# Kernel tuning notes

Hardware: AMD Instinct MI355X
Metric: run time of the kernel (lower is better)

Reference implementation:

```python
import jax, jax.numpy as jnp
import numpy as np

N = 50000      # nodes
E = 800000     # edges (before self loops)
F_IN = 50      # PPI num_features
H = 4          # heads
C = 64         # hidden per head
NC = 121       # PPI num_classes
NEG_SLOPE = 0.2


def setup_inputs() -> dict:
    key = jax.random.key(0)
    ks = jax.random.split(key, 20)
    p = lambda k, shape: (jax.random.normal(k, shape, jnp.float32) * 0.1)
    x0 = jax.random.normal(ks[0], (N, F_IN), jnp.float32)
    edge_index = jax.random.randint(ks[1], (2, E), 0, N, dtype=jnp.int64)
    return dict(
        x0=x0, edge_index=edge_index,
        W1=p(ks[2], (F_IN, H * C)), as1=p(ks[3], (H, C)), ad1=p(ks[4], (H, C)),
        res1=p(ks[5], (F_IN, H * C)), b1=jnp.zeros((H * C,), jnp.float32),
        W2=p(ks[6], (H * C, H * C)), as2=p(ks[7], (H, C)), ad2=p(ks[8], (H, C)),
        res2=p(ks[9], (H * C, H * C)), b2=jnp.zeros((H * C,), jnp.float32),
        W3=p(ks[10], (H * C, H * NC)), as3=p(ks[11], (H, NC)), ad3=p(ks[12], (H, NC)),
        res3=p(ks[13], (H * C, NC)), b3=jnp.zeros((NC,), jnp.float32),
    )


def _gat(x, src, dst, W, a_src, a_dst, resW, b, concat):
    """PyG-style GATConv with residual, self loops already in (src, dst)."""
    n = x.shape[0]
    heads, outc = a_src.shape
    h = (x @ W).reshape(n, heads, outc)                 # [N,H,C]
    al_s = (h * a_src).sum(-1)                          # [N,H]
    al_d = (h * a_dst).sum(-1)                          # [N,H]
    e = jax.nn.leaky_relu(al_s[src] + al_d[dst], NEG_SLOPE)  # [E,H]
    m = jax.ops.segment_max(e, dst, num_segments=n)     # stable softmax per dst
    ex = jnp.exp(e - m[dst])
    denom = jax.ops.segment_sum(ex, dst, num_segments=n)
    alpha = ex / denom[dst]                             # [E,H]
    out = jax.ops.segment_sum(h[src] * alpha[:, :, None], dst, num_segments=n)  # [N,H,C]
    out = out.reshape(n, heads * outc) if concat else out.mean(axis=1)
    return out + x @ resW + b


def reference(x0, edge_index,
              W1, as1, ad1, res1, b1,
              W2, as2, ad2, res2, b2,
              W3, as3, ad3, res3, b3):
    n = x0.shape[0]
    loop = jnp.arange(n, dtype=edge_index.dtype)        # add self loops (PyG default)
    src = jnp.concatenate([edge_index[0], loop])
    dst = jnp.concatenate([edge_index[1], loop])
    x1 = jax.nn.relu(_gat(x0, src, dst, W1, as1, ad1, res1, b1, True))
    x2 = jax.nn.relu(_gat(x1, src, dst, W2, as2, ad2, res2, b2, True))
    x3 = _gat(x2, src, dst, W3, as3, ad3, res3, b3, False)
    return x3
```

## Files before the change

kernel.cpp:

```cpp
#include <hip/hip_runtime.h>

#define NNODES 50000
#define NEDGES 800000
#define NTOT   (NEDGES + NNODES)
#define F_IN   50
#define KPAD1  64
#define HEADS  4
#define C1     64
#define HC1    256
#define NC     121
#define K1S    320
#define K3S    1280
#define N2S    512
#define N2X    520
#define SLOTS  128

typedef unsigned short ushort_t;
typedef __attribute__((ext_vector_type(4))) unsigned short ushort4_t;
typedef __attribute__((ext_vector_type(8))) unsigned short ushort8;
typedef __attribute__((ext_vector_type(8))) __bf16 bf16x8;
typedef __attribute__((ext_vector_type(4))) float f32x4;
typedef __attribute__((ext_vector_type(4))) int int4_t;

__device__ __forceinline__ ushort_t f2bf(float f) {
    union { float f; unsigned int u; } v; v.f = f;
    unsigned int u = v.u;
    return (ushort_t)((u + 0x7fffu + ((u >> 16) & 1u)) >> 16);
}
__device__ __forceinline__ float bf2f(ushort_t s) {
    union { unsigned int u; float f; } v; v.u = ((unsigned int)s) << 16;
    return v.f;
}
__device__ __forceinline__ float lrelu(float x) { return x > 0.f ? x : 0.2f * x; }
__device__ __forceinline__ f32x4 cvt4lo(ushort8 v) {
    f32x4 r; r[0] = bf2f(v[0]); r[1] = bf2f(v[1]); r[2] = bf2f(v[2]); r[3] = bf2f(v[3]);
    return r;
}
__device__ __forceinline__ f32x4 cvt4hi(ushort8 v) {
    f32x4 r; r[0] = bf2f(v[4]); r[1] = bf2f(v[5]); r[2] = bf2f(v[6]); r[3] = bf2f(v[7]);
    return r;
}
__device__ __forceinline__ void wave_lds_sync() {
    asm volatile("s_waitcnt lgkmcnt(0)" ::: "memory");
}

__device__ __forceinline__ void scatter_body4(int i0, const int* __restrict__ ei,
                                              int* __restrict__ cnt,
                                              int* __restrict__ csr_src) {
    #pragma unroll
    for (int u = 0; u < 4; ++u) {
        int i = i0 + u * 256;
        if (i >= NTOT) continue;
        int s, d;
        if (i < NEDGES) { s = ei[i]; d = ei[NEDGES + i]; }
        else            { s = d = i - NEDGES; }
        if ((unsigned)d >= NNODES) d = 0;
        if ((unsigned)s >= NNODES) s = 0;
        int k = atomicAdd(&cnt[d], 1);
        if (k < SLOTS) csr_src[d * SLOTS + k] = s;
    }
}

#define SZ_A (NNODES * KPAD1)
#define SZ_B (HC1 * K1S)
#define SZ_C (N2X * HC1)
#define SZ_D (N2X)
#define SZ_E (NC * K3S)
#define SZ_G (HC1 * 4)
#define PREP_TOTAL (SZ_A + SZ_B + SZ_C + SZ_D + SZ_E + 2 * SZ_G)
#define PREP_BLK ((PREP_TOTAL + 255) / 256)
#define SCAT_BLK ((NTOT + 1023) / 1024)
#define GEMV1_BLK (NNODES / 8)

__device__ void prep_body(int i,
                 const float* __restrict__ x0,
                 const float* __restrict__ W1, const float* __restrict__ res1,
                 const float* __restrict__ W2, const float* __restrict__ res2,
                 const float* __restrict__ W3, const float* __restrict__ res3,
                 const float* __restrict__ as2, const float* __restrict__ ad2,
                 const float* __restrict__ as3, const float* __restrict__ ad3,
                 const float* __restrict__ b2,
                 ushort_t* __restrict__ x0b, ushort_t* __restrict__ Bt1,
                 ushort_t* __restrict__ Bt2, ushort_t* __restrict__ Bt3,
                 float* __restrict__ bias520,
                 float* __restrict__ w_as3, float* __restrict__ w_ad3) {
    if (i < SZ_A) {
        int m = i >> 6, k = i & 63;
        x0b[i] = (k < F_IN) ? f2bf(x0[(size_t)m * F_IN + k]) : (ushort_t)0;
        return;
    }
    i -= SZ_A;
    if (i < SZ_B) {
        int c = i / K1S, kk = i - c * K1S;
        float v = 0.f;
        if (kk < 256) {
            int h = kk >> 6, k = kk & 63;
            if (k < F_IN && (c >> 6) == h) v = W1[(size_t)k * HC1 + c];
        } else {
            int k = kk - 256;
            if (k < F_IN) v = res1[(size_t)k * HC1 + c];
        }
        Bt1[i] = f2bf(v);
        return;
    }
    i -= SZ_B;
    if (i < SZ_C) {
        int c = i / HC1, k = i - c * HC1;
        float v;
        if (c < HC1) {
            v = W2[(size_t)k * HC1 + c];
        } else if (c < 512) {
            v = res2[(size_t)k * HC1 + (c - HC1)];
        } else {
            int j = c - 512;
            int h = j & 3;
            const float* a = (j < 4) ? as2 : ad2;
            float s = 0.f;
            for (int cc = 0; cc < C1; ++cc)
                s += W2[(size_t)k * HC1 + h * C1 + cc] * a[h * C1 + cc];
            v = s;
        }
        Bt2[i] = f2bf(v);
        return;
    }
    i -= SZ_C;
    if (i < SZ_D) {
        bias520[i] = (i >= HC1 && i < 512) ? b2[i - HC1] : 0.f;
        return;
    }
    i -= SZ_D;
    if (i < SZ_E) {
        int c = i / K3S, kk = i - c * K3S;
        float v;
        if (kk < 1024) {
            int h = kk >> 8, k = kk & 255;
            v = 0.25f * W3[(size_t)k * (HEADS * NC) + h * NC + c];
        } else {
            int k = kk - 1024;
            v = res3[(size_t)k * NC + c];
        }
        Bt3[i] = f2bf(v);
        return;
    }
    i -= SZ_E;
    {
        int grp = i / SZ_G, ii = i - grp * SZ_G;
        int k = ii >> 2, h = ii & 3;
        const float* a = grp ? ad3 : as3;
        float s = 0.f;
        for (int c = 0; c < NC; ++c)
            s += W3[(size_t)k * (HEADS * NC) + h * NC + c] * a[h * NC + c];
        (grp ? w_ad3 : w_as3)[ii] = s;
    }
}

__device__ void gemv1_body(int b, int tid,
                           const float* __restrict__ x0,
                           const float* __restrict__ W1,
                           const float* __restrict__ as1, const float* __restrict__ ad1,
                           float* __restrict__ als, float* __restrict__ ald,
                           float* lds_w ) {
    int k = tid >> 2, h = tid & 3;
    float s = 0.f, sd = 0.f;
    if (k < F_IN) {
        for (int c = 0; c < C1; ++c) {
            float wv = W1[(size_t)k * HC1 + h * C1 + c];
            s  += wv * as1[h * C1 + c];
            sd += wv * ad1[h * C1 + c];
        }
    }
    lds_w[k * 8 + h] = s;
    lds_w[k * 8 + 4 + h] = sd;
    __syncthreads();
    int wid = tid >> 6, lane = tid & 63;
    #pragma unroll
    for (int t = 0; t < 2; ++t) {
        int n = b * 8 + wid * 2 + t;
        float xv = (lane < F_IN) ? x0[(size_t)n * F_IN + lane] : 0.f;
        f32x4 was = *(const f32x4*)&lds_w[lane * 8];
        f32x4 wad = *(const f32x4*)&lds_w[lane * 8 + 4];
        f32x4 ps = xv * was, pd = xv * wad;
        #pragma unroll
        for (int off = 32; off; off >>= 1)
            #pragma unroll
            for (int hh = 0; hh < HEADS; ++hh) {
                ps[hh] += __shfl_xor(ps[hh], off);
                pd[hh] += __shfl_xor(pd[hh], off);
            }
        if (lane == 0) {
            *(f32x4*)&als[n * 4] = ps;
            *(f32x4*)&ald[n * 4] = pd;
        }
    }
}

__global__ __launch_bounds__(256)
void prep_scatter_gemv_kernel(const float* __restrict__ x0,
                 const float* __restrict__ W1, const float* __restrict__ res1,
                 const float* __restrict__ W2, const float* __restrict__ res2,
                 const float* __restrict__ W3, const float* __restrict__ res3,
                 const float* __restrict__ as1, const float* __restrict__ ad1,
                 const float* __restrict__ as2, const float* __restrict__ ad2,
                 const float* __restrict__ as3, const float* __restrict__ ad3,
                 const float* __restrict__ b2,
                 ushort_t* __restrict__ x0b, ushort_t* __restrict__ Bt1,
                 ushort_t* __restrict__ Bt2, ushort_t* __restrict__ Bt3,
                 float* __restrict__ bias520,
                 float* __restrict__ w_as3, float* __restrict__ w_ad3,
                 const int* __restrict__ ei, int* __restrict__ cnt,
                 int* __restrict__ csr_src,
                 float* __restrict__ als, float* __restrict__ ald) {
    __shared__ float lds_w[64 * 8];
    int b = blockIdx.x;
    if (b < PREP_BLK) {
        prep_body(b * 256 + threadIdx.x, x0, W1, res1, W2, res2, W3, res3,
                  as2, ad2, as3, ad3, b2, x0b, Bt1, Bt2, Bt3,
                  bias520, w_as3, w_ad3);
    } else if (b < PREP_BLK + SCAT_BLK) {
        scatter_body4((b - PREP_BLK) * 1024 + threadIdx.x, ei, cnt, csr_src);
    } else {
        gemv1_body(b - PREP_BLK - SCAT_BLK, threadIdx.x, x0, W1, as1, ad1,
                   als, ald, lds_w);
    }
}

#define BM 128
#define BN 128
#define BK 64
#define LDP (BK + 8)

__global__ __launch_bounds__(256)
void gemm_mfma_kernel(const ushort_t* __restrict__ A1, int lda1,
                      const ushort_t* __restrict__ A2, int lda2, int Ksplit,
                      const ushort_t* __restrict__ Bt, const float* __restrict__ bias,
                      ushort_t* __restrict__ Cb,
                      int M, int N, int K, int relu) {
    __shared__ ushort_t As[BM * LDP];
    __shared__ ushort_t Bs[BN * LDP];
    int tid = threadIdx.x;
    int lane = tid & 63;
    int wid = tid >> 6;
    int wm = (wid & 1) * 64, wn = (wid >> 1) * 64;
    int l15 = lane & 15;
    int q8 = (lane >> 4) * 8;
    int m0 = blockIdx.y * BM, n0 = blockIdx.x * BN;

    f32x4 acc[4][4] = {};

    for (int k0 = 0; k0 < K; k0 += BK) {
        #pragma unroll
        for (int it = 0; it < 4; ++it) {
            int c = tid + it * 256;
            int row = c >> 3, c8 = c & 7;
            int k = k0 + c8 * 8;
            ushort8 va = (ushort8)0;
            int gm = m0 + row;
            if (gm < M) {
                if (k < Ksplit) va = *(const ushort8*)&A1[(size_t)gm * lda1 + k];
                else            va = *(const ushort8*)&A2[(size_t)gm * lda2 + (k - Ksplit)];
            }
            *(ushort8*)&As[row * LDP + c8 * 8] = va;
            ushort8 vb = (ushort8)0;
            int gn = n0 + row;
            if (gn < N) vb = *(const ushort8*)&Bt[(size_t)gn * K + k];
            *(ushort8*)&Bs[row * LDP + c8 * 8] = vb;
        }
        __syncthreads();
        #pragma unroll
        for (int kk = 0; kk < BK; kk += 32) {
            bf16x8 af[4], bfr[4];
            #pragma unroll
            for (int mi = 0; mi < 4; ++mi)
                af[mi] = *(const bf16x8*)&As[(wm + mi * 16 + l15) * LDP + kk + q8];
            #pragma unroll
            for (int ni = 0; ni < 4; ++ni)
                bfr[ni] = *(const bf16x8*)&Bs[(wn + ni * 16 + l15) * LDP + kk + q8];
            #pragma unroll
            for (int mi = 0; mi < 4; ++mi)
                #pragma unroll
                for (int ni = 0; ni < 4; ++ni)
                    acc[mi][ni] = __builtin_amdgcn_mfma_f32_16x16x32_bf16(
                        af[mi], bfr[ni], acc[mi][ni], 0, 0, 0);
        }
        __syncthreads();
    }

    #pragma unroll
    for (int mi = 0; mi < 4; ++mi) {
        int mbase = m0 + wm + mi * 16 + (lane >> 4) * 4;
        #pragma unroll
        for (int ni = 0; ni < 4; ++ni) {
            int ncol = n0 + wn + ni * 16 + l15;
            if (ncol >= N) continue;
            float bv = bias ? bias[ncol] : 0.f;
            #pragma unroll
            for (int r = 0; r < 4; ++r) {
                int m = mbase + r;
                if (m >= M) continue;
                float v = acc[mi][ni][r] + bv;
                if (relu) v = fmaxf(v, 0.f);
                Cb[(size_t)m * N + ncol] = f2bf(v);
            }
        }
    }
}

__global__ __launch_bounds__(256)
void gemm2x_kernel(const ushort_t* __restrict__ A,
                   const ushort_t* __restrict__ Bt,
                   const float* __restrict__ bias,
                   ushort_t* __restrict__ comb,
                   float* __restrict__ als, float* __restrict__ ald,
                   int M) {
    __shared__ ushort_t As[BM * LDP];
    __shared__ ushort_t Bs[BN * LDP];
    int tid = threadIdx.x;
    int lane = tid & 63;
    int wid = tid >> 6;
    int wm = (wid & 1) * 64, wn = (wid >> 1) * 64;
    int l15 = lane & 15;
    int q8 = (lane >> 4) * 8;
    int m0 = blockIdx.y * BM, n0 = blockIdx.x * BN;

    f32x4 acc[4][4] = {};

    for (int k0 = 0; k0 < HC1; k0 += BK) {
        #pragma unroll
        for (int it = 0; it < 4; ++it) {
            int c = tid + it * 256;
            int row = c >> 3, c8 = c & 7;
            int k = k0 + c8 * 8;
            ushort8 va = (ushort8)0;
            int gm = m0 + row;
            if (gm < M) va = *(const ushort8*)&A[(size_t)gm * HC1 + k];
            *(ushort8*)&As[row * LDP + c8 * 8] = va;
            ushort8 vb = (ushort8)0;
            int gn = n0 + row;
            if (gn < N2X) vb = *(const ushort8*)&Bt[(size_t)gn * HC1 + k];
            *(ushort8*)&Bs[row * LDP + c8 * 8] = vb;
        }
        __syncthreads();
        #pragma unroll
        for (int kk = 0; kk < BK; kk += 32) {
            bf16x8 af[4], bfr[4];
            #pragma unroll
            for (int mi = 0; mi < 4; ++mi)
                af[mi] = *(const bf16x8*)&As[(wm + mi * 16 + l15) * LDP + kk + q8];
            #pragma unroll
            for (int ni = 0; ni < 4; ++ni)
                bfr[ni] = *(const bf16x8*)&Bs[(wn + ni * 16 + l15) * LDP + kk + q8];
            #pragma unroll
            for (int mi = 0; mi < 4; ++mi)
                #pragma unroll
                for (int ni = 0; ni < 4; ++ni)
                    acc[mi][ni] = __builtin_amdgcn_mfma_f32_16x16x32_bf16(
                        af[mi], bfr[ni], acc[mi][ni], 0, 0, 0);
        }
        __syncthreads();
    }

    #pragma unroll
    for (int mi = 0; mi < 4; ++mi) {
        int mbase = m0 + wm + mi * 16 + (lane >> 4) * 4;
        #pragma unroll
        for (int ni = 0; ni < 4; ++ni) {
            int ncol = n0 + wn + ni * 16 + l15;
            if (ncol >= N2X) continue;
            float bv = bias[ncol];
            #pragma unroll
            for (int r = 0; r < 4; ++r) {
                int m = mbase + r;
                if (m >= M) continue;
                float v = acc[mi][ni][r] + bv;
                if (ncol < 512) {
                    comb[(size_t)m * N2S + ncol] = f2bf(v);
                } else {
                    int j = ncol - 512;
                    if (j < 4) als[m * 4 + j] = v;
                    else       ald[m * 4 + (j - 4)] = v;
                }
            }
        }
    }
}

__global__ __launch_bounds__(256)
void gemm3s_kernel(const ushort_t* __restrict__ A1, int lda1,
                   const ushort_t* __restrict__ A2, int lda2, int Ksplit,
                   const ushort_t* __restrict__ Bt, const float* __restrict__ bias,
                   float* __restrict__ out, int M, int N, int K) {
    __shared__ ushort_t As[64 * LDP];
    __shared__ ushort_t Bs[128 * LDP];
    int tid = threadIdx.x, lane = tid & 63, wid = tid >> 6;
    int l15 = lane & 15, q8 = (lane >> 4) * 8;
    int m0 = blockIdx.x * 64;
    f32x4 c4[8] = {};
    for (int k0 = 0; k0 < K; k0 += BK) {
        #pragma unroll
        for (int it = 0; it < 2; ++it) {
            int c = tid + it * 256;
            int row = c >> 3, c8 = c & 7;
            int k = k0 + c8 * 8;
            ushort8 va = (ushort8)0;
            int gm = m0 + row;
            if (gm < M) {
                if (k < Ksplit) va = *(const ushort8*)&A1[(size_t)gm * lda1 + k];
                else            va = *(const ushort8*)&A2[(size_t)gm * lda2 + (k - Ksplit)];
            }
            *(ushort8*)&As[row * LDP + c8 * 8] = va;
        }
        #pragma unroll
        for (int it = 0; it < 4; ++it) {
            int c = tid + it * 256;
            int row = c >> 3, c8 = c & 7;
            int k = k0 + c8 * 8;
            ushort8 vb = (ushort8)0;
            if (row < N) vb = *(const ushort8*)&Bt[(size_t)row * K + k];
            *(ushort8*)&Bs[row * LDP + c8 * 8] = vb;
        }
        __syncthreads();
        #pragma unroll
        for (int kk = 0; kk < BK; kk += 32) {
            bf16x8 af = *(const bf16x8*)&As[(wid * 16 + l15) * LDP + kk + q8];
            #pragma unroll
            for (int ni = 0; ni < 8; ++ni) {
                bf16x8 bf = *(const bf16x8*)&Bs[(ni * 16 + l15) * LDP + kk + q8];
                c4[ni] = __builtin_amdgcn_mfma_f32_16x16x32_bf16(af, bf, c4[ni], 0, 0, 0);
            }
        }
        __syncthreads();
    }
    int rbase = m0 + wid * 16 + (lane >> 4) * 4;
    #pragma unroll
    for (int ni = 0; ni < 8; ++ni) {
        int col = ni * 16 + l15;
        if (col >= NC) continue;
        float bv = bias[col];
        #pragma unroll
        for (int r = 0; r < 4; ++r) {
            int m = rbase + r;
            if (m < M) out[(size_t)m * NC + col] = c4[ni][r] + bv;
        }
    }
}

#define E_CHUNK32(ROWBYTES)                                                   \
    int i = base + l;                                                         \
    int nv = end - base; if (nv > 32) nv = 32;                                \
    if (i < end) {                                                            \
        int s = csr_src[i];                                                   \
        soffw[l] = s * (ROWBYTES);                                            \
        f32x4 av = *(const f32x4*)&als[s * 4];                                \
        f32x4 e;                                                              \
        _Pragma("unroll")                                                     \
        for (int h = 0; h < HEADS; ++h) {                                     \
            e[h] = __expf(lrelu(av[h] + aldd[h]));                            \
            den4[h] += e[h];                                                  \
        }                                                                     \
        *(f32x4*)&sew[l * 4] = e;                                             \
    }                                                                         \
    wave_lds_sync();

#define DEN_REDUCE16                                                          \
    _Pragma("unroll")                                                         \
    for (int off = 16; off; off >>= 1)                                        \
        _Pragma("unroll")                                                     \
        for (int h = 0; h < HEADS; ++h)                                       \
            den4[h] += __shfl_xor(den4[h], off);

__global__ __launch_bounds__(256)
void agg1_kernel(const ushort_t* __restrict__ x0b,
                 const float* __restrict__ als, const float* __restrict__ ald,
                 const int* __restrict__ cnt, const int* __restrict__ csr_src,
                 ushort_t* __restrict__ aggx) {
    __shared__ int   soff[8][32];
    __shared__ float se[8][32 * 4];
    int tid = threadIdx.x;
    int hw = tid >> 5, l = tid & 31;
    int d = blockIdx.x * 8 + hw;
    int* soffw = soff[hw];
    float* sew = se[hw];
    int beg = d * SLOTS;
    int deg = cnt[d]; if (deg > SLOTS) deg = SLOTS;
    int end = beg + deg;
    f32x4 aldd = *(const f32x4*)&ald[d * 4];
    f32x4 den4 = (f32x4)0.f;
    f32x4 acc0 = (f32x4)0.f, acc1 = (f32x4)0.f;
    int lb = l * 4;
    for (int base = beg; base < end; base += 32) {
        E_CHUNK32(KPAD1 * 2)
        int j = 0;
        for (; j + 4 <= nv; j += 4) {
            int4_t o = *(const int4_t*)&soffw[j];
            f32x4 e0 = *(const f32x4*)&sew[j * 4];
            f32x4 e1 = *(const f32x4*)&sew[(j + 1) * 4];
            f32x4 e2 = *(const f32x4*)&sew[(j + 2) * 4];
            f32x4 e3 = *(const f32x4*)&sew[(j + 3) * 4];
            unsigned int v0 = *(const unsigned int*)((const char*)x0b + o.x + lb);
            unsigned int v1 = *(const unsigned int*)((const char*)x0b + o.y + lb);
            unsigned int v2 = *(const unsigned int*)((const char*)x0b + o.z + lb);
            unsigned int v3 = *(const unsigned int*)((const char*)x0b + o.w + lb);
            acc0 += e0 * bf2f((ushort_t)(v0 & 0xffffu)) + e1 * bf2f((ushort_t)(v1 & 0xffffu))
                  + e2 * bf2f((ushort_t)(v2 & 0xffffu)) + e3 * bf2f((ushort_t)(v3 & 0xffffu));
            acc1 += e0 * bf2f((ushort_t)(v0 >> 16)) + e1 * bf2f((ushort_t)(v1 >> 16))
                  + e2 * bf2f((ushort_t)(v2 >> 16)) + e3 * bf2f((ushort_t)(v3 >> 16));
        }
        for (; j < nv; ++j) {
            int o = soffw[j];
            f32x4 e = *(const f32x4*)&sew[j * 4];
            unsigned int v = *(const unsigned int*)((const char*)x0b + o + lb);
            acc0 += e * bf2f((ushort_t)(v & 0xffffu));
            acc1 += e * bf2f((ushort_t)(v >> 16));
        }
        wave_lds_sync();
    }
    DEN_REDUCE16
    #pragma unroll
    for (int h = 0; h < HEADS; ++h) {
        float r = 1.f / den4[h];
        unsigned int pk = (unsigned int)f2bf(acc0[h] * r)
                        | ((unsigned int)f2bf(acc1[h] * r) << 16);
        *(unsigned int*)&aggx[(size_t)d * HC1 + h * 64 + l * 2] = pk;
    }
}

__global__ __launch_bounds__(256)
void agg2_kernel(const ushort_t* __restrict__ comb,
                 const float* __restrict__ als, const float* __restrict__ ald,
                 const int* __restrict__ cnt, const int* __restrict__ csr_src,
                 const float* __restrict__ w_as3, const float* __restrict__ w_ad3,
                 ushort_t* __restrict__ xnext,
                 float* __restrict__ als3, float* __restrict__ ald3) {
    __shared__ int   soff[8][32];
    __shared__ float se[8][32 * 4];
    int tid = threadIdx.x;
    int hw = tid >> 5, l = tid & 31;
    int d = blockIdx.x * 8 + hw;
    int* soffw = soff[hw];
    float* sew = se[hw];
    int hh = l >> 3;
    int beg = d * SLOTS;
    int deg = cnt[d]; if (deg > SLOTS) deg = SLOTS;
    int end = beg + deg;
    f32x4 aldd = *(const f32x4*)&ald[d * 4];
    f32x4 den4 = (f32x4)0.f;
    f32x4 acc[2] = {};
    int lb = l * 16;
    for (int base = beg; base < end; base += 32) {
        E_CHUNK32(N2S * 2)
        int j = 0;
        for (; j + 4 <= nv; j += 4) {
            int4_t o = *(const int4_t*)&soffw[j];
            ushort8 v0 = *(const ushort8*)((const char*)comb + o.x + lb);
            ushort8 v1 = *(const ushort8*)((const char*)comb + o.y + lb);
            ushort8 v2 = *(const ushort8*)((const char*)comb + o.z + lb);
            ushort8 v3 = *(const ushort8*)((const char*)comb + o.w + lb);
            float e0 = sew[j * 4 + hh], e1 = sew[(j + 1) * 4 + hh];
            float e2 = sew[(j + 2) * 4 + hh], e3 = sew[(j + 3) * 4 + hh];
            acc[0] += e0 * cvt4lo(v0) + e1 * cvt4lo(v1) + e2 * cvt4lo(v2) + e3 * cvt4lo(v3);
            acc[1] += e0 * cvt4hi(v0) + e1 * cvt4hi(v1) + e2 * cvt4hi(v2) + e3 * cvt4hi(v3);
        }
        for (; j < nv; ++j) {
            int o = soffw[j];
            float e = sew[j * 4 + hh];
            ushort8 v = *(const ushort8*)((const char*)comb + o + lb);
            acc[0] += e * cvt4lo(v);
            acc[1] += e * cvt4hi(v);
        }
        wave_lds_sync();
    }
    DEN_REDUCE16
    float r = 1.f / den4[hh];
    ushort8 rv = *(const ushort8*)&comb[(size_t)d * N2S + 256 + l * 8];
    float vout[8];
    ushort8 o8;
    #pragma unroll
    for (int q = 0; q < 2; ++q)
        #pragma unroll
        for (int c = 0; c < 4; ++c) {
            float vv = fmaxf(acc[q][c] * r + bf2f(rv[q * 4 + c]), 0.f);
            vout[q * 4 + c] = vv;
            o8[q * 4 + c] = f2bf(vv);
        }
    *(ushort8*)&xnext[(size_t)d * HC1 + l * 8] = o8;
    f32x4 ps = (f32x4)0.f, pd = (f32x4)0.f;
    #pragma unroll
    for (int cc = 0; cc < 8; ++cc) {
        int col = l * 8 + cc;
        f32x4 wsj = *(const f32x4*)&w_as3[col * 4];
        f32x4 wdj = *(const f32x4*)&w_ad3[col * 4];
        ps += vout[cc] * wsj;
        pd += vout[cc] * wdj;
    }
    #pragma unroll
    for (int off = 16; off; off >>= 1) {
        #pragma unroll
        for (int h = 0; h < HEADS; ++h) {
            ps[h] += __shfl_xor(ps[h], off);
            pd[h] += __shfl_xor(pd[h], off);
        }
    }
    if (l == 0) {
        *(f32x4*)&als3[d * 4] = ps;
        *(f32x4*)&ald3[d * 4] = pd;
    }
}

__global__ __launch_bounds__(256)
void agg3_kernel(const ushort_t* __restrict__ x2b,
                 const float* __restrict__ als, const float* __restrict__ ald,
                 const int* __restrict__ cnt, const int* __restrict__ csr_src,
                 ushort_t* __restrict__ aggx) {
    __shared__ int   soff[8][32];
    __shared__ float se[8][32 * 4];
    int tid = threadIdx.x;
    int hw = tid >> 5, l = tid & 31;
    int d = blockIdx.x * 8 + hw;
    int* soffw = soff[hw];
    float* sew = se[hw];
    int beg = d * SLOTS;
    int deg = cnt[d]; if (deg > SLOTS) deg = SLOTS;
    int end = beg + deg;
    f32x4 aldd = *(const f32x4*)&ald[d * 4];
    f32x4 den4 = (f32x4)0.f;
    f32x4 acc[HEADS][2] = {};
    int lb = l * 16;
    for (int base = beg; base < end; base += 32) {
        E_CHUNK32(HC1 * 2)
        int j = 0;
        for (; j + 4 <= nv; j += 4) {
            int4_t o = *(const int4_t*)&soffw[j];
            ushort8 v0 = *(const ushort8*)((const char*)x2b + o.x + lb);
            ushort8 v1 = *(const ushort8*)((const char*)x2b + o.y + lb);
            ushort8 v2 = *(const ushort8*)((const char*)x2b + o.z + lb);
            ushort8 v3 = *(const ushort8*)((const char*)x2b + o.w + lb);
            f32x4 e0 = *(const f32x4*)&sew[j * 4];
            f32x4 e1 = *(const f32x4*)&sew[(j + 1) * 4];
            f32x4 e2 = *(const f32x4*)&sew[(j + 2) * 4];
            f32x4 e3 = *(const f32x4*)&sew[(j + 3) * 4];
            f32x4 xl, xh;
            xl = cvt4lo(v0); xh = cvt4hi(v0);
            #pragma unroll
            for (int h = 0; h < HEADS; ++h) { acc[h][0] += e0[h] * xl; acc[h][1] += e0[h] * xh; }
            xl = cvt4lo(v1); xh = cvt4hi(v1);
            #pragma unroll
            for (int h = 0; h < HEADS; ++h) { acc[h][0] += e1[h] * xl; acc[h][1] += e1[h] * xh; }
            xl = cvt4lo(v2); xh = cvt4hi(v2);
            #pragma unroll
            for (int h = 0; h < HEADS; ++h) { acc[h][0] += e2[h] * xl; acc[h][1] += e2[h] * xh; }
            xl = cvt4lo(v3); xh = cvt4hi(v3);
            #pragma unroll
            for (int h = 0; h < HEADS; ++h) { acc[h][0] += e3[h] * xl; acc[h][1] += e3[h] * xh; }
        }
        for (; j < nv; ++j) {
            int o = soffw[j];
            f32x4 e = *(const f32x4*)&sew[j * 4];
            ushort8 v = *(const ushort8*)((const char*)x2b + o + lb);
            f32x4 xl = cvt4lo(v), xh = cvt4hi(v);
            #pragma unroll
            for (int h = 0; h < HEADS; ++h) { acc[h][0] += e[h] * xl; acc[h][1] += e[h] * xh; }
        }
        wave_lds_sync();
    }
    DEN_REDUCE16
    #pragma unroll
    for (int h = 0; h < HEADS; ++h) {
        float rdv = 1.f / den4[h];
        ushort8 ow;
        #pragma unroll
        for (int q = 0; q < 2; ++q)
            #pragma unroll
            for (int c = 0; c < 4; ++c)
                ow[q * 4 + c] = f2bf(acc[h][q][c] * rdv);
        *(ushort8*)&aggx[(size_t)d * 1024 + h * HC1 + l * 8] = ow;
    }
}

extern "C" void kernel_launch(void* const* d_in, const int* in_sizes, int n_in,
                              void* d_out, int out_size, void* d_ws, size_t ws_size,
                              hipStream_t stream) {
    const float* x0   = (const float*)d_in[0];
    const int*   ei   = (const int*)d_in[1];
    const float* W1   = (const float*)d_in[2];
    const float* as1  = (const float*)d_in[3];
    const float* ad1  = (const float*)d_in[4];
    const float* res1 = (const float*)d_in[5];
    const float* b1   = (const float*)d_in[6];
    const float* W2   = (const float*)d_in[7];
    const float* as2  = (const float*)d_in[8];
    const float* ad2  = (const float*)d_in[9];
    const float* res2 = (const float*)d_in[10];
    const float* b2   = (const float*)d_in[11];
    const float* W3   = (const float*)d_in[12];
    const float* as3  = (const float*)d_in[13];
    const float* ad3  = (const float*)d_in[14];
    const float* res3 = (const float*)d_in[15];
    const float* b3   = (const float*)d_in[16];

    char* p = (char*)d_ws;
    auto alloc = [&](size_t bytes) -> void* {
        void* r = (void*)p;
        p += (bytes + 255) & ~(size_t)255;
        return r;
    };
    int*      cnt     = (int*)alloc((size_t)NNODES * 4);
    int*      csr_src = (int*)alloc((size_t)NNODES * SLOTS * 4);
    float*    als     = (float*)alloc((size_t)NNODES * HEADS * 4);
    float*    ald     = (float*)alloc((size_t)NNODES * HEADS * 4);
    float*    als3    = (float*)alloc((size_t)NNODES * HEADS * 4);
    float*    ald3    = (float*)alloc((size_t)NNODES * HEADS * 4);
    ushort_t* x0b     = (ushort_t*)alloc((size_t)NNODES * KPAD1 * 2);
    ushort_t* x2      = (ushort_t*)alloc((size_t)NNODES * HC1 * 2);
    ushort_t* Bt1     = (ushort_t*)alloc((size_t)HC1 * K1S * 2);
    ushort_t* Bt2     = (ushort_t*)alloc((size_t)N2X * HC1 * 2);
    float*    bias520 = (float*)alloc((size_t)N2X * 4);
    ushort_t* Bt3     = (ushort_t*)alloc((size_t)NC * K3S * 2);
    float*    w_as3   = (float*)alloc((size_t)HC1 * 4 * 4);
    float*    w_ad3   = (float*)alloc((size_t)HC1 * 4 * 4);
    char*     big     = (char*)alloc((size_t)NNODES * 1024 * 2);
    ushort_t* aggx1   = (ushort_t*)big;
    ushort_t* x1      = (ushort_t*)(big + (size_t)NNODES * HC1 * 2);
    ushort_t* comb    = (ushort_t*)(big + (size_t)NNODES * HC1 * 4);
    ushort_t* aggx3   = (ushort_t*)big;

    hipMemsetAsync(cnt, 0, (size_t)NNODES * 4, stream);

    prep_scatter_gemv_kernel<<<PREP_BLK + SCAT_BLK + GEMV1_BLK, 256, 0, stream>>>(
        x0, W1, res1, W2, res2, W3, res3, as1, ad1, as2, ad2, as3, ad3, b2,
        x0b, Bt1, Bt2, Bt3, bias520, w_as3, w_ad3,
        ei, cnt, csr_src, als, ald);

    int nagg8 = NNODES / 8;

    agg1_kernel<<<nagg8, 256, 0, stream>>>(x0b, als, ald, cnt, csr_src, aggx1);
    {
        dim3 g((HC1 + BN - 1) / BN, (NNODES + BM - 1) / BM);
        gemm_mfma_kernel<<<g, 256, 0, stream>>>(aggx1, HC1, x0b, KPAD1, HC1,
                                                Bt1, b1, x1, NNODES, HC1, K1S, 1);
    }

    {
        dim3 g((N2X + BN - 1) / BN, (NNODES + BM - 1) / BM);
        gemm2x_kernel<<<g, 256, 0, stream>>>(x1, Bt2, bias520, comb, als, ald, NNODES);
    }
    agg2_kernel<<<nagg8, 256, 0, stream>>>(comb, als, ald, cnt, csr_src,
                                           w_as3, w_ad3, x2, als3, ald3);

    agg3_kernel<<<nagg8, 256, 0, stream>>>(x2, als3, ald3, cnt, csr_src, aggx3);
    gemm3s_kernel<<<(NNODES + 63) / 64, 256, 0, stream>>>(
        aggx3, 1024, x2, HC1, 1024, Bt3, b3, (float*)d_out, NNODES, 128, K3S);
}
```

Measured before the change: 623.2 us.

## Split layer-1 logit GEMV into own kernel and process two nodes per half-wave

```diff
diff --git a/kernel.cpp b/kernel.cpp
--- a/kernel.cpp
+++ b/kernel.cpp
@@ -44,21 +44,17 @@
     asm volatile("s_waitcnt lgkmcnt(0)" ::: "memory");
 }
 
-__device__ __forceinline__ void scatter_body4(int i0, const int* __restrict__ ei,
-                                              int* __restrict__ cnt,
-                                              int* __restrict__ csr_src) {
-    #pragma unroll
-    for (int u = 0; u < 4; ++u) {
-        int i = i0 + u * 256;
-        if (i >= NTOT) continue;
-        int s, d;
-        if (i < NEDGES) { s = ei[i]; d = ei[NEDGES + i]; }
-        else            { s = d = i - NEDGES; }
-        if ((unsigned)d >= NNODES) d = 0;
-        if ((unsigned)s >= NNODES) s = 0;
-        int k = atomicAdd(&cnt[d], 1);
-        if (k < SLOTS) csr_src[d * SLOTS + k] = s;
-    }
+__device__ __forceinline__ void scatter_body(int i, const int* __restrict__ ei,
+                                             int* __restrict__ cnt,
+                                             int* __restrict__ csr_src) {
+    if (i >= NTOT) return;
+    int s, d;
+    if (i < NEDGES) { s = ei[i]; d = ei[NEDGES + i]; }
+    else            { s = d = i - NEDGES; }
+    if ((unsigned)d >= NNODES) d = 0;
+    if ((unsigned)s >= NNODES) s = 0;
+    int k = atomicAdd(&cnt[d], 1);
+    if (k < SLOTS) csr_src[d * SLOTS + k] = s;
 }
 
 #define SZ_A (NNODES * KPAD1)
@@ -66,23 +62,25 @@
 #define SZ_C (N2X * HC1)
 #define SZ_D (N2X)
 #define SZ_E (NC * K3S)
+#define SZ_F (KPAD1 * 4)
 #define SZ_G (HC1 * 4)
-#define PREP_TOTAL (SZ_A + SZ_B + SZ_C + SZ_D + SZ_E + 2 * SZ_G)
+#define PREP_TOTAL (SZ_A + SZ_B + SZ_C + SZ_D + SZ_E + 2 * SZ_F + 2 * SZ_G)
 #define PREP_BLK ((PREP_TOTAL + 255) / 256)
-#define SCAT_BLK ((NTOT + 1023) / 1024)
-#define GEMV1_BLK (NNODES / 8)
+#define CNT_BLK  ((NTOT + 255) / 256)
 
 __device__ void prep_body(int i,
                  const float* __restrict__ x0,
                  const float* __restrict__ W1, const float* __restrict__ res1,
                  const float* __restrict__ W2, const float* __restrict__ res2,
                  const float* __restrict__ W3, const float* __restrict__ res3,
+                 const float* __restrict__ as1, const float* __restrict__ ad1,
                  const float* __restrict__ as2, const float* __restrict__ ad2,
                  const float* __restrict__ as3, const float* __restrict__ ad3,
                  const float* __restrict__ b2,
                  ushort_t* __restrict__ x0b, ushort_t* __restrict__ Bt1,
                  ushort_t* __restrict__ Bt2, ushort_t* __restrict__ Bt3,
                  float* __restrict__ bias520,
+                 float* __restrict__ w_as1, float* __restrict__ w_ad1,
                  float* __restrict__ w_as3, float* __restrict__ w_ad3) {
     if (i < SZ_A) {
         int m = i >> 6, k = i & 63;
@@ -143,6 +141,18 @@
         return;
     }
     i -= SZ_E;
+    if (i < 2 * SZ_F) {
+        const float* a = (i < SZ_F) ? as1 : ad1;
+        float* w = (i < SZ_F) ? w_as1 : w_ad1;
+        int ii = (i < SZ_F) ? i : i - SZ_F;
+        int k = ii >> 2, h = ii & 3;
+        float s = 0.f;
+        if (k < F_IN)
+            for (int c = 0; c < C1; ++c) s += W1[(size_t)k * HC1 + h * C1 + c] * a[h * C1 + c];
+        w[ii] = s;
+        return;
+    }
+    i -= 2 * SZ_F;
     {
         int grp = i / SZ_G, ii = i - grp * SZ_G;
         int k = ii >> 2, h = ii & 3;
@@ -154,48 +164,8 @@
     }
 }
 
-__device__ void gemv1_body(int b, int tid,
-                           const float* __restrict__ x0,
-                           const float* __restrict__ W1,
-                           const float* __restrict__ as1, const float* __restrict__ ad1,
-                           float* __restrict__ als, float* __restrict__ ald,
-                           float* lds_w ) {
-    int k = tid >> 2, h = tid & 3;
-    float s = 0.f, sd = 0.f;
-    if (k < F_IN) {
-        for (int c = 0; c < C1; ++c) {
-            float wv = W1[(size_t)k * HC1 + h * C1 + c];
-            s  += wv * as1[h * C1 + c];
-            sd += wv * ad1[h * C1 + c];
-        }
-    }
-    lds_w[k * 8 + h] = s;
-    lds_w[k * 8 + 4 + h] = sd;
-    __syncthreads();
-    int wid = tid >> 6, lane = tid & 63;
-    #pragma unroll
-    for (int t = 0; t < 2; ++t) {
-        int n = b * 8 + wid * 2 + t;
-        float xv = (lane < F_IN) ? x0[(size_t)n * F_IN + lane] : 0.f;
-        f32x4 was = *(const f32x4*)&lds_w[lane * 8];
-        f32x4 wad = *(const f32x4*)&lds_w[lane * 8 + 4];
-        f32x4 ps = xv * was, pd = xv * wad;
-        #pragma unroll
-        for (int off = 32; off; off >>= 1)
-            #pragma unroll
-            for (int hh = 0; hh < HEADS; ++hh) {
-                ps[hh] += __shfl_xor(ps[hh], off);
-                pd[hh] += __shfl_xor(pd[hh], off);
-            }
-        if (lane == 0) {
-            *(f32x4*)&als[n * 4] = ps;
-            *(f32x4*)&ald[n * 4] = pd;
-        }
-    }
-}
-
 __global__ __launch_bounds__(256)
-void prep_scatter_gemv_kernel(const float* __restrict__ x0,
+void prep_scatter_kernel(const float* __restrict__ x0,
                  const float* __restrict__ W1, const float* __restrict__ res1,
                  const float* __restrict__ W2, const float* __restrict__ res2,
                  const float* __restrict__ W3, const float* __restrict__ res3,
@@ -206,21 +176,17 @@
                  ushort_t* __restrict__ x0b, ushort_t* __restrict__ Bt1,
                  ushort_t* __restrict__ Bt2, ushort_t* __restrict__ Bt3,
                  float* __restrict__ bias520,
+                 float* __restrict__ w_as1, float* __restrict__ w_ad1,
                  float* __restrict__ w_as3, float* __restrict__ w_ad3,
                  const int* __restrict__ ei, int* __restrict__ cnt,
-                 int* __restrict__ csr_src,
-                 float* __restrict__ als, float* __restrict__ ald) {
-    __shared__ float lds_w[64 * 8];
+                 int* __restrict__ csr_src) {
     int b = blockIdx.x;
     if (b < PREP_BLK) {
         prep_body(b * 256 + threadIdx.x, x0, W1, res1, W2, res2, W3, res3,
-                  as2, ad2, as3, ad3, b2, x0b, Bt1, Bt2, Bt3,
-                  bias520, w_as3, w_ad3);
-    } else if (b < PREP_BLK + SCAT_BLK) {
-        scatter_body4((b - PREP_BLK) * 1024 + threadIdx.x, ei, cnt, csr_src);
+                  as1, ad1, as2, ad2, as3, ad3, b2, x0b, Bt1, Bt2, Bt3,
+                  bias520, w_as1, w_ad1, w_as3, w_ad3);
     } else {
-        gemv1_body(b - PREP_BLK - SCAT_BLK, threadIdx.x, x0, W1, as1, ad1,
-                   als, ald, lds_w);
+        scatter_body((b - PREP_BLK) * 256 + threadIdx.x, ei, cnt, csr_src);
     }
 }
 
@@ -444,6 +410,40 @@
     }
 }
 
+__global__ __launch_bounds__(256)
+void logits_gemv_kernel(const ushort_t* __restrict__ X, int K,
+                        const float* __restrict__ w_as, const float* __restrict__ w_ad,
+                        float* __restrict__ als, float* __restrict__ ald) {
+    int wid = threadIdx.x >> 6, lane = threadIdx.x & 63;
+    int n = blockIdx.x * 4 + wid;
+    float ps[HEADS] = {}, pd[HEADS] = {};
+    for (int k0 = lane * 4; k0 < K; k0 += 256) {
+        ushort4_t xv = *(const ushort4_t*)&X[(size_t)n * K + k0];
+        float x[4] = {bf2f(xv.x), bf2f(xv.y), bf2f(xv.z), bf2f(xv.w)};
+        #pragma unroll
+        for (int j = 0; j < 4; ++j) {
+            #pragma unroll
+            for (int h = 0; h < HEADS; ++h) {
+                ps[h] += x[j] * w_as[(k0 + j) * 4 + h];
+                pd[h] += x[j] * w_ad[(k0 + j) * 4 + h];
+            }
+        }
+    }
+    #pragma unroll
+    for (int off = 32; off; off >>= 1)
+        #pragma unroll
+        for (int h = 0; h < HEADS; ++h) {
+            ps[h] += __shfl_xor(ps[h], off);
+            pd[h] += __shfl_xor(pd[h], off);
+        }
+    if (lane == 0)
+        #pragma unroll
+        for (int h = 0; h < HEADS; ++h) {
+            als[n * HEADS + h] = ps[h];
+            ald[n * HEADS + h] = pd[h];
+        }
+}
+
 #define E_CHUNK32(ROWBYTES)                                                   \
     int i = base + l;                                                         \
     int nv = end - base; if (nv > 32) nv = 32;                                \
@@ -468,6 +468,7 @@
         for (int h = 0; h < HEADS; ++h)                                       \
             den4[h] += __shfl_xor(den4[h], off);
 
+
 __global__ __launch_bounds__(256)
 void agg1_kernel(const ushort_t* __restrict__ x0b,
                  const float* __restrict__ als, const float* __restrict__ ald,
@@ -477,50 +478,53 @@
     __shared__ float se[8][32 * 4];
     int tid = threadIdx.x;
     int hw = tid >> 5, l = tid & 31;
-    int d = blockIdx.x * 8 + hw;
     int* soffw = soff[hw];
     float* sew = se[hw];
-    int beg = d * SLOTS;
-    int deg = cnt[d]; if (deg > SLOTS) deg = SLOTS;
-    int end = beg + deg;
-    f32x4 aldd = *(const f32x4*)&ald[d * 4];
-    f32x4 den4 = (f32x4)0.f;
-    f32x4 acc0 = (f32x4)0.f, acc1 = (f32x4)0.f;
     int lb = l * 4;
-    for (int base = beg; base < end; base += 32) {
-        E_CHUNK32(KPAD1 * 2)
-        int j = 0;
-        for (; j + 4 <= nv; j += 4) {
-            int4_t o = *(const int4_t*)&soffw[j];
-            f32x4 e0 = *(const f32x4*)&sew[j * 4];
-            f32x4 e1 = *(const f32x4*)&sew[(j + 1) * 4];
-            f32x4 e2 = *(const f32x4*)&sew[(j + 2) * 4];
-            f32x4 e3 = *(const f32x4*)&sew[(j + 3) * 4];
-            unsigned int v0 = *(const unsigned int*)((const char*)x0b + o.x + lb);
-            unsigned int v1 = *(const unsigned int*)((const char*)x0b + o.y + lb);
-            unsigned int v2 = *(const unsigned int*)((const char*)x0b + o.z + lb);
-            unsigned int v3 = *(const unsigned int*)((const char*)x0b + o.w + lb);
-            acc0 += e0 * bf2f((ushort_t)(v0 & 0xffffu)) + e1 * bf2f((ushort_t)(v1 & 0xffffu))
-                  + e2 * bf2f((ushort_t)(v2 & 0xffffu)) + e3 * bf2f((ushort_t)(v3 & 0xffffu));
-            acc1 += e0 * bf2f((ushort_t)(v0 >> 16)) + e1 * bf2f((ushort_t)(v1 >> 16))
-                  + e2 * bf2f((ushort_t)(v2 >> 16)) + e3 * bf2f((ushort_t)(v3 >> 16));
-        }
-        for (; j < nv; ++j) {
-            int o = soffw[j];
-            f32x4 e = *(const f32x4*)&sew[j * 4];
-            unsigned int v = *(const unsigned int*)((const char*)x0b + o + lb);
-            acc0 += e * bf2f((ushort_t)(v & 0xffffu));
-            acc1 += e * bf2f((ushort_t)(v >> 16));
-        }
-        wave_lds_sync();
-    }
-    DEN_REDUCE16
     #pragma unroll
-    for (int h = 0; h < HEADS; ++h) {
-        float r = 1.f / den4[h];
-        unsigned int pk = (unsigned int)f2bf(acc0[h] * r)
-                        | ((unsigned int)f2bf(acc1[h] * r) << 16);
-        *(unsigned int*)&aggx[(size_t)d * HC1 + h * 64 + l * 2] = pk;
+    for (int rr = 0; rr < 2; ++rr) {
+        int d = blockIdx.x * 16 + hw * 2 + rr;
+        int beg = d * SLOTS;
+        int deg = cnt[d]; if (deg > SLOTS) deg = SLOTS;
+        int end = beg + deg;
+        f32x4 aldd = *(const f32x4*)&ald[d * 4];
+        f32x4 den4 = (f32x4)0.f;
+        f32x4 acc0 = (f32x4)0.f, acc1 = (f32x4)0.f;
+        for (int base = beg; base < end; base += 32) {
+            E_CHUNK32(KPAD1 * 2)
+            int j = 0;
+            for (; j + 4 <= nv; j += 4) {
+                int4_t o = *(const int4_t*)&soffw[j];
+                f32x4 e0 = *(const f32x4*)&sew[j * 4];
+                f32x4 e1 = *(const f32x4*)&sew[(j + 1) * 4];
+                f32x4 e2 = *(const f32x4*)&sew[(j + 2) * 4];
+                f32x4 e3 = *(const f32x4*)&sew[(j + 3) * 4];
+                unsigned int v0 = *(const unsigned int*)((const char*)x0b + o.x + lb);
+                unsigned int v1 = *(const unsigned int*)((const char*)x0b + o.y + lb);
+                unsigned int v2 = *(const unsigned int*)((const char*)x0b + o.z + lb);
+                unsigned int v3 = *(const unsigned int*)((const char*)x0b + o.w + lb);
+                acc0 += e0 * bf2f((ushort_t)(v0 & 0xffffu)) + e1 * bf2f((ushort_t)(v1 & 0xffffu))
+                      + e2 * bf2f((ushort_t)(v2 & 0xffffu)) + e3 * bf2f((ushort_t)(v3 & 0xffffu));
+                acc1 += e0 * bf2f((ushort_t)(v0 >> 16)) + e1 * bf2f((ushort_t)(v1 >> 16))
+                      + e2 * bf2f((ushort_t)(v2 >> 16)) + e3 * bf2f((ushort_t)(v3 >> 16));
+            }
+            for (; j < nv; ++j) {
+                int o = soffw[j];
+                f32x4 e = *(const f32x4*)&sew[j * 4];
+                unsigned int v = *(const unsigned int*)((const char*)x0b + o + lb);
+                acc0 += e * bf2f((ushort_t)(v & 0xffffu));
+                acc1 += e * bf2f((ushort_t)(v >> 16));
+            }
+            wave_lds_sync();
+        }
+        DEN_REDUCE16
+        #pragma unroll
+        for (int h = 0; h < HEADS; ++h) {
+            float r = 1.f / den4[h];
+            unsigned int pk = (unsigned int)f2bf(acc0[h] * r)
+                            | ((unsigned int)f2bf(acc1[h] * r) << 16);
+            *(unsigned int*)&aggx[(size_t)d * HC1 + h * 64 + l * 2] = pk;
+        }
     }
 }
 
@@ -535,74 +539,77 @@
     __shared__ float se[8][32 * 4];
     int tid = threadIdx.x;
     int hw = tid >> 5, l = tid & 31;
-    int d = blockIdx.x * 8 + hw;
     int* soffw = soff[hw];
     float* sew = se[hw];
     int hh = l >> 3;
-    int beg = d * SLOTS;
-    int deg = cnt[d]; if (deg > SLOTS) deg = SLOTS;
-    int end = beg + deg;
-    f32x4 aldd = *(const f32x4*)&ald[d * 4];
-    f32x4 den4 = (f32x4)0.f;
-    f32x4 acc[2] = {};
     int lb = l * 16;
-    for (int base = beg; base < end; base += 32) {
-        E_CHUNK32(N2S * 2)
-        int j = 0;
-        for (; j + 4 <= nv; j += 4) {
-            int4_t o = *(const int4_t*)&soffw[j];
-            ushort8 v0 = *(const ushort8*)((const char*)comb + o.x + lb);
-            ushort8 v1 = *(const ushort8*)((const char*)comb + o.y + lb);
-            ushort8 v2 = *(const ushort8*)((const char*)comb + o.z + lb);
-            ushort8 v3 = *(const ushort8*)((const char*)comb + o.w + lb);
-            float e0 = sew[j * 4 + hh], e1 = sew[(j + 1) * 4 + hh];
-            float e2 = sew[(j + 2) * 4 + hh], e3 = sew[(j + 3) * 4 + hh];
-            acc[0] += e0 * cvt4lo(v0) + e1 * cvt4lo(v1) + e2 * cvt4lo(v2) + e3 * cvt4lo(v3);
-            acc[1] += e0 * cvt4hi(v0) + e1 * cvt4hi(v1) + e2 * cvt4hi(v2) + e3 * cvt4hi(v3);
-        }
-        for (; j < nv; ++j) {
-            int o = soffw[j];
-            float e = sew[j * 4 + hh];
-            ushort8 v = *(const ushort8*)((const char*)comb + o + lb);
-            acc[0] += e * cvt4lo(v);
-            acc[1] += e * cvt4hi(v);
-        }
-        wave_lds_sync();
-    }
-    DEN_REDUCE16
-    float r = 1.f / den4[hh];
-    ushort8 rv = *(const ushort8*)&comb[(size_t)d * N2S + 256 + l * 8];
-    float vout[8];
-    ushort8 o8;
     #pragma unroll
-    for (int q = 0; q < 2; ++q)
-        #pragma unroll
-        for (int c = 0; c < 4; ++c) {
-            float vv = fmaxf(acc[q][c] * r + bf2f(rv[q * 4 + c]), 0.f);
-            vout[q * 4 + c] = vv;
-            o8[q * 4 + c] = f2bf(vv);
-        }
-    *(ushort8*)&xnext[(size_t)d * HC1 + l * 8] = o8;
-    f32x4 ps = (f32x4)0.f, pd = (f32x4)0.f;
-    #pragma unroll
-    for (int cc = 0; cc < 8; ++cc) {
-        int col = l * 8 + cc;
-        f32x4 wsj = *(const f32x4*)&w_as3[col * 4];
-        f32x4 wdj = *(const f32x4*)&w_ad3[col * 4];
-        ps += vout[cc] * wsj;
-        pd += vout[cc] * wdj;
-    }
-    #pragma unroll
-    for (int off = 16; off; off >>= 1) {
-        #pragma unroll
-        for (int h = 0; h < HEADS; ++h) {
-            ps[h] += __shfl_xor(ps[h], off);
-            pd[h] += __shfl_xor(pd[h], off);
-        }
-    }
-    if (l == 0) {
-        *(f32x4*)&als3[d * 4] = ps;
-        *(f32x4*)&ald3[d * 4] = pd;
+    for (int rr = 0; rr < 2; ++rr) {
+        int d = blockIdx.x * 16 + hw * 2 + rr;
+        int beg = d * SLOTS;
+        int deg = cnt[d]; if (deg > SLOTS) deg = SLOTS;
+        int end = beg + deg;
+        f32x4 aldd = *(const f32x4*)&ald[d * 4];
+        f32x4 den4 = (f32x4)0.f;
+        f32x4 acc[2] = {};
+        for (int base = beg; base < end; base += 32) {
+            E_CHUNK32(N2S * 2)
+            int j = 0;
+            for (; j + 4 <= nv; j += 4) {
+                int4_t o = *(const int4_t*)&soffw[j];
+                ushort8 v0 = *(const ushort8*)((const char*)comb + o.x + lb);
+                ushort8 v1 = *(const ushort8*)((const char*)comb + o.y + lb);
+                ushort8 v2 = *(const ushort8*)((const char*)comb + o.z + lb);
+                ushort8 v3 = *(const ushort8*)((const char*)comb + o.w + lb);
+                float e0 = sew[j * 4 + hh], e1 = sew[(j + 1) * 4 + hh];
+                float e2 = sew[(j + 2) * 4 + hh], e3 = sew[(j + 3) * 4 + hh];
+                acc[0] += e0 * cvt4lo(v0) + e1 * cvt4lo(v1) + e2 * cvt4lo(v2) + e3 * cvt4lo(v3);
+                acc[1] += e0 * cvt4hi(v0) + e1 * cvt4hi(v1) + e2 * cvt4hi(v2) + e3 * cvt4hi(v3);
+            }
+            for (; j < nv; ++j) {
+                int o = soffw[j];
+                float e = sew[j * 4 + hh];
+                ushort8 v = *(const ushort8*)((const char*)comb + o + lb);
+                acc[0] += e * cvt4lo(v);
+                acc[1] += e * cvt4hi(v);
+            }
+            wave_lds_sync();
+        }
+        DEN_REDUCE16
+        float r = 1.f / den4[hh];
+        ushort8 rv = *(const ushort8*)&comb[(size_t)d * N2S + 256 + l * 8];
+        float vout[8];
+        ushort8 o8;
+        #pragma unroll
+        for (int q = 0; q < 2; ++q)
+            #pragma unroll
+            for (int c = 0; c < 4; ++c) {
+                float vv = fmaxf(acc[q][c] * r + bf2f(rv[q * 4 + c]), 0.f);
+                vout[q * 4 + c] = vv;
+                o8[q * 4 + c] = f2bf(vv);
+            }
+        *(ushort8*)&xnext[(size_t)d * HC1 + l * 8] = o8;
+        f32x4 ps = (f32x4)0.f, pd = (f32x4)0.f;
+        #pragma unroll
+        for (int cc = 0; cc < 8; ++cc) {
+            int col = l * 8 + cc;
+            f32x4 wsj = *(const f32x4*)&w_as3[col * 4];
+            f32x4 wdj = *(const f32x4*)&w_ad3[col * 4];
+            ps += vout[cc] * wsj;
+            pd += vout[cc] * wdj;
+        }
+        #pragma unroll
+        for (int off = 16; off; off >>= 1) {
+            #pragma unroll
+            for (int h = 0; h < HEADS; ++h) {
+                ps[h] += __shfl_xor(ps[h], off);
+                pd[h] += __shfl_xor(pd[h], off);
+            }
+        }
+        if (l == 0) {
+            *(f32x4*)&als3[d * 4] = ps;
+            *(f32x4*)&ald3[d * 4] = pd;
+        }
     }
 }
 
@@ -615,64 +622,67 @@
     __shared__ float se[8][32 * 4];
     int tid = threadIdx.x;
     int hw = tid >> 5, l = tid & 31;
-    int d = blockIdx.x * 8 + hw;
     int* soffw = soff[hw];
     float* sew = se[hw];
-    int beg = d * SLOTS;
-    int deg = cnt[d]; if (deg > SLOTS) deg = SLOTS;
-    int end = beg + deg;
-    f32x4 aldd = *(const f32x4*)&ald[d * 4];
-    f32x4 den4 = (f32x4)0.f;
-    f32x4 acc[HEADS][2] = {};
     int lb = l * 16;
-    for (int base = beg; base < end; base += 32) {
-        E_CHUNK32(HC1 * 2)
-        int j = 0;
-        for (; j + 4 <= nv; j += 4) {
-            int4_t o = *(const int4_t*)&soffw[j];
-            ushort8 v0 = *(const ushort8*)((const char*)x2b + o.x + lb);
-            ushort8 v1 = *(const ushort8*)((const char*)x2b + o.y + lb);
-            ushort8 v2 = *(const ushort8*)((const char*)x2b + o.z + lb);
-            ushort8 v3 = *(const ushort8*)((const char*)x2b + o.w + lb);
-            f32x4 e0 = *(const f32x4*)&sew[j * 4];
-            f32x4 e1 = *(const f32x4*)&sew[(j + 1) * 4];
-            f32x4 e2 = *(const f32x4*)&sew[(j + 2) * 4];
-            f32x4 e3 = *(const f32x4*)&sew[(j + 3) * 4];
-            f32x4 xl, xh;
-            xl = cvt4lo(v0); xh = cvt4hi(v0);
-            #pragma unroll
-            for (int h = 0; h < HEADS; ++h) { acc[h][0] += e0[h] * xl; acc[h][1] += e0[h] * xh; }
-            xl = cvt4lo(v1); xh = cvt4hi(v1);
-            #pragma unroll
-            for (int h = 0; h < HEADS; ++h) { acc[h][0] += e1[h] * xl; acc[h][1] += e1[h] * xh; }
-            xl = cvt4lo(v2); xh = cvt4hi(v2);
-            #pragma unroll
-            for (int h = 0; h < HEADS; ++h) { acc[h][0] += e2[h] * xl; acc[h][1] += e2[h] * xh; }
-            xl = cvt4lo(v3); xh = cvt4hi(v3);
-            #pragma unroll
-            for (int h = 0; h < HEADS; ++h) { acc[h][0] += e3[h] * xl; acc[h][1] += e3[h] * xh; }
-        }
-        for (; j < nv; ++j) {
-            int o = soffw[j];
-            f32x4 e = *(const f32x4*)&sew[j * 4];
-            ushort8 v = *(const ushort8*)((const char*)x2b + o + lb);
-            f32x4 xl = cvt4lo(v), xh = cvt4hi(v);
-            #pragma unroll
-            for (int h = 0; h < HEADS; ++h) { acc[h][0] += e[h] * xl; acc[h][1] += e[h] * xh; }
-        }
-        wave_lds_sync();
-    }
-    DEN_REDUCE16
     #pragma unroll
-    for (int h = 0; h < HEADS; ++h) {
-        float rdv = 1.f / den4[h];
-        ushort8 ow;
-        #pragma unroll
-        for (int q = 0; q < 2; ++q)
-            #pragma unroll
-            for (int c = 0; c < 4; ++c)
-                ow[q * 4 + c] = f2bf(acc[h][q][c] * rdv);
-        *(ushort8*)&aggx[(size_t)d * 1024 + h * HC1 + l * 8] = ow;
+    for (int rr = 0; rr < 2; ++rr) {
+        int d = blockIdx.x * 16 + hw * 2 + rr;
+        int beg = d * SLOTS;
+        int deg = cnt[d]; if (deg > SLOTS) deg = SLOTS;
+        int end = beg + deg;
+        f32x4 aldd = *(const f32x4*)&ald[d * 4];
+        f32x4 den4 = (f32x4)0.f;
+        f32x4 acc[HEADS][2] = {};
+        for (int base = beg; base < end; base += 32) {
+            E_CHUNK32(HC1 * 2)
+            int j = 0;
+            for (; j + 4 <= nv; j += 4) {
+                int4_t o = *(const int4_t*)&soffw[j];
+                ushort8 v0 = *(const ushort8*)((const char*)x2b + o.x + lb);
+                ushort8 v1 = *(const ushort8*)((const char*)x2b + o.y + lb);
+                ushort8 v2 = *(const ushort8*)((const char*)x2b + o.z + lb);
+                ushort8 v3 = *(const ushort8*)((const char*)x2b + o.w + lb);
+                f32x4 e0 = *(const f32x4*)&sew[j * 4];
+                f32x4 e1 = *(const f32x4*)&sew[(j + 1) * 4];
+                f32x4 e2 = *(const f32x4*)&sew[(j + 2) * 4];
+                f32x4 e3 = *(const f32x4*)&sew[(j + 3) * 4];
+                f32x4 xl, xh;
+                xl = cvt4lo(v0); xh = cvt4hi(v0);
+                #pragma unroll
+                for (int h = 0; h < HEADS; ++h) { acc[h][0] += e0[h] * xl; acc[h][1] += e0[h] * xh; }
+                xl = cvt4lo(v1); xh = cvt4hi(v1);
+                #pragma unroll
+                for (int h = 0; h < HEADS; ++h) { acc[h][0] += e1[h] * xl; acc[h][1] += e1[h] * xh; }
+                xl = cvt4lo(v2); xh = cvt4hi(v2);
+                #pragma unroll
+                for (int h = 0; h < HEADS; ++h) { acc[h][0] += e2[h] * xl; acc[h][1] += e2[h] * xh; }
+                xl = cvt4lo(v3); xh = cvt4hi(v3);
+                #pragma unroll
+                for (int h = 0; h < HEADS; ++h) { acc[h][0] += e3[h] * xl; acc[h][1] += e3[h] * xh; }
+            }
+            for (; j < nv; ++j) {
+                int o = soffw[j];
+                f32x4 e = *(const f32x4*)&sew[j * 4];
+                ushort8 v = *(const ushort8*)((const char*)x2b + o + lb);
+                f32x4 xl = cvt4lo(v), xh = cvt4hi(v);
+                #pragma unroll
+                for (int h = 0; h < HEADS; ++h) { acc[h][0] += e[h] * xl; acc[h][1] += e[h] * xh; }
+            }
+            wave_lds_sync();
+        }
+        DEN_REDUCE16
+        #pragma unroll
+        for (int h = 0; h < HEADS; ++h) {
+            float rdv = 1.f / den4[h];
+            ushort8 ow;
+            #pragma unroll
+            for (int q = 0; q < 2; ++q)
+                #pragma unroll
+                for (int c = 0; c < 4; ++c)
+                    ow[q * 4 + c] = f2bf(acc[h][q][c] * rdv);
+            *(ushort8*)&aggx[(size_t)d * 1024 + h * HC1 + l * 8] = ow;
+        }
     }
 }
 
@@ -715,6 +725,8 @@
     ushort_t* Bt2     = (ushort_t*)alloc((size_t)N2X * HC1 * 2);
     float*    bias520 = (float*)alloc((size_t)N2X * 4);
     ushort_t* Bt3     = (ushort_t*)alloc((size_t)NC * K3S * 2);
+    float*    w_as1   = (float*)alloc((size_t)KPAD1 * 4 * 4);
+    float*    w_ad1   = (float*)alloc((size_t)KPAD1 * 4 * 4);
     float*    w_as3   = (float*)alloc((size_t)HC1 * 4 * 4);
     float*    w_ad3   = (float*)alloc((size_t)HC1 * 4 * 4);
     char*     big     = (char*)alloc((size_t)NNODES * 1024 * 2);
@@ -725,14 +737,16 @@
 
     hipMemsetAsync(cnt, 0, (size_t)NNODES * 4, stream);
 
-    prep_scatter_gemv_kernel<<<PREP_BLK + SCAT_BLK + GEMV1_BLK, 256, 0, stream>>>(
+    prep_scatter_kernel<<<PREP_BLK + CNT_BLK, 256, 0, stream>>>(
         x0, W1, res1, W2, res2, W3, res3, as1, ad1, as2, ad2, as3, ad3, b2,
-        x0b, Bt1, Bt2, Bt3, bias520, w_as3, w_ad3,
-        ei, cnt, csr_src, als, ald);
-
-    int nagg8 = NNODES / 8;
-
-    agg1_kernel<<<nagg8, 256, 0, stream>>>(x0b, als, ald, cnt, csr_src, aggx1);
+        x0b, Bt1, Bt2, Bt3, bias520, w_as1, w_ad1, w_as3, w_ad3,
+        ei, cnt, csr_src);
+
+    int nagg4  = NNODES / 4;
+    int nagg16 = NNODES / 16;
+
+    logits_gemv_kernel<<<nagg4, 256, 0, stream>>>(x0b, KPAD1, w_as1, w_ad1, als, ald);
+    agg1_kernel<<<nagg16, 256, 0, stream>>>(x0b, als, ald, cnt, csr_src, aggx1);
     {
         dim3 g((HC1 + BN - 1) / BN, (NNODES + BM - 1) / BM);
         gemm_mfma_kernel<<<g, 256, 0, stream>>>(aggx1, HC1, x0b, KPAD1, HC1,
@@ -743,10 +757,10 @@
         dim3 g((N2X + BN - 1) / BN, (NNODES + BM - 1) / BM);
         gemm2x_kernel<<<g, 256, 0, stream>>>(x1, Bt2, bias520, comb, als, ald, NNODES);
     }
-    agg2_kernel<<<nagg8, 256, 0, stream>>>(comb, als, ald, cnt, csr_src,
-                                           w_as3, w_ad3, x2, als3, ald3);
-
-    agg3_kernel<<<nagg8, 256, 0, stream>>>(x2, als3, ald3, cnt, csr_src, aggx3);
+    agg2_kernel<<<nagg16, 256, 0, stream>>>(comb, als, ald, cnt, csr_src,
+                                            w_as3, w_ad3, x2, als3, ald3);
+
+    agg3_kernel<<<nagg16, 256, 0, stream>>>(x2, als3, ald3, cnt, csr_src, aggx3);
     gemm3s_kernel<<<(NNODES + 63) / 64, 256, 0, stream>>>(
         aggx3, 1024, x2, HC1, 1024, Bt3, b3, (float*)d_out, NNODES, 128, K3S);
 }
```

Result: faster. 584.0 us (-6.3%).
